# Optimization experiments

Hardware: AMD Instinct MI355X
Metric: run time of the kernel (lower is better)

Reference implementation:

```python
import jax, jax.numpy as jnp
import numpy as np

T, H = 1024, 2048          # tokens, hidden size
E, F = 32, 1408            # routed experts, expert intermediate
G, TOPK_G, TOPK = 8, 3, 6  # expert groups, top groups, top-k experts
FS = 2 * F                 # shared-expert intermediate (n_shared_experts=2)
SCALE = 16.0               # routed_scaling_factor


def setup_inputs() -> dict:
    key = jax.random.key(0)
    ks = jax.random.split(key, 6)
    s = 0.02
    return {
        "hidden_states": jax.random.normal(ks[0], (T, H), jnp.float32),
        "w_gate": jax.random.normal(ks[1], (E, H), jnp.float32) * s,
        "w1": jax.random.normal(ks[2], (E, H, 2 * F), jnp.float32) * s,   # gate_up per expert
        "w2": jax.random.normal(ks[3], (E, F, H), jnp.float32) * s,       # down per expert
        "ws1": jax.random.normal(ks[4], (H, 2 * FS), jnp.float32) * s,    # shared gate_up
        "ws2": jax.random.normal(ks[5], (FS, H), jnp.float32) * s,        # shared down
    }


def _grouped_topk(scores):
    # scores: [T, E] softmax probs. DeepSeek grouped top-k routing.
    g_scores = scores.reshape(T, G, E // G).max(axis=-1)          # [T, G]
    _, g_idx = jax.lax.top_k(g_scores, TOPK_G)                    # [T, TOPK_G]
    g_mask = jnp.zeros((T, G), scores.dtype).at[
        jnp.arange(T)[:, None], g_idx].set(1.0)                   # [T, G]
    score_mask = jnp.repeat(g_mask, E // G, axis=1)               # [T, E]
    masked = scores * score_mask                                  # masked_fill(0)
    topk_w, topk_ids = jax.lax.top_k(masked, TOPK)                # [T, TOPK]
    # norm_topk_prob=False -> no renormalization
    return topk_w, topk_ids


def reference(hidden_states, w_gate, w1, w2, ws1, ws2):
    x = hidden_states  # [T, H]

    # shared experts MLP (SiluAndMul)
    gu_s = x @ ws1                                   # [T, 2*FS]
    shared = (jax.nn.silu(gu_s[:, :FS]) * gu_s[:, FS:]) @ ws2  # [T, H]

    # router
    logits = x @ w_gate.T                            # [T, E]
    scores = jax.nn.softmax(logits, axis=-1)
    topk_w, topk_ids = _grouped_topk(scores)

    # combine weights as dense [T, E] (reference-dense expert execution)
    comb = jnp.zeros((T, E), x.dtype).at[
        jnp.arange(T)[:, None], topk_ids].add(topk_w)

    gu = jnp.einsum('th,ehf->tef', x, w1)            # [T, E, 2F]
    act = jax.nn.silu(gu[..., :F]) * gu[..., F:]     # [T, E, F]
    routed = jnp.einsum('tef,efh,te->th', act, w2, comb)  # weighted combine

    return routed * SCALE + shared
```

## Files before the change

### kernel.cpp

```cpp
#include <hip/hip_runtime.h>
#include <hip/hip_bf16.h>

#define T_TOK 1024
#define H_DIM 2048
#define E_NUM 32
#define F_DIM 1408
#define G_NUM 8
#define TOPKG 3
#define TOPK  6
#define FS_DIM 2816
#define SCALE_F 16.0f

#define BM 128
#define BK 32
#define LDP 40

typedef __attribute__((ext_vector_type(8))) __bf16 bf16x8;
typedef __attribute__((ext_vector_type(4))) float f32x4;

__device__ __forceinline__ unsigned short f2bf(float f) {
    union { float f; unsigned u; } v; v.f = f;
    unsigned r = v.u + 0x7fffu + ((v.u >> 16) & 1u);
    return (unsigned short)(r >> 16);
}

__device__ __forceinline__ bf16x8 ld_frag(const unsigned short* p) {
    union { uint4 u; bf16x8 v; } x;
    x.u = *(const uint4*)p;
    return x.v;
}

__device__ __forceinline__ f32x4 mfma16(bf16x8 a, bf16x8 b, f32x4 c) {
    return __builtin_amdgcn_mfma_f32_16x16x32_bf16(a, b, c, 0, 0, 0);
}

__global__ void prep_kernel(const float* __restrict__ x, unsigned short* __restrict__ xb,
                            int* __restrict__ cnt, int* __restrict__ cnt2) {
    if (blockIdx.x == 0) {
        if (threadIdx.x < E_NUM) cnt[threadIdx.x] = 0;
        else if (threadIdx.x < 2 * E_NUM) cnt2[threadIdx.x - E_NUM] = 0;
    }
    int i = blockIdx.x * blockDim.x + threadIdx.x;
    float4 v = ((const float4*)x)[i];
    uint2 o;
    o.x = (unsigned)f2bf(v.x) | ((unsigned)f2bf(v.y) << 16);
    o.y = (unsigned)f2bf(v.z) | ((unsigned)f2bf(v.w) << 16);
    ((uint2*)xb)[i] = o;
}

__global__ void router_kernel(const float* __restrict__ x, const float* __restrict__ wg,
                              float* __restrict__ topk_w, int* __restrict__ topk_ids,
                              int* __restrict__ cnt) {
    int t = blockIdx.x;
    __shared__ float xs[H_DIM];
    __shared__ float logits[E_NUM];
    const float* xr = x + (size_t)t * H_DIM;
    for (int i = threadIdx.x; i < H_DIM / 4; i += 256)
        ((float4*)xs)[i] = ((const float4*)xr)[i];
    __syncthreads();
    int wave = threadIdx.x >> 6, lane = threadIdx.x & 63;
    for (int eo = 0; eo < 8; ++eo) {
        int e = wave * 8 + eo;
        const float* w = wg + (size_t)e * H_DIM;
        float s = 0.f;
        for (int i = lane; i < H_DIM; i += 64) s += xs[i] * w[i];
        for (int d = 32; d; d >>= 1) s += __shfl_down(s, d);
        if (lane == 0) logits[e] = s;
    }
    __syncthreads();
    if (threadIdx.x == 0) {
        float sc[E_NUM];
        float mx = -1e30f;
        for (int e = 0; e < E_NUM; ++e) mx = fmaxf(mx, logits[e]);
        float sum = 0.f;
        for (int e = 0; e < E_NUM; ++e) { sc[e] = expf(logits[e] - mx); sum += sc[e]; }
        float inv = 1.0f / sum;
        for (int e = 0; e < E_NUM; ++e) sc[e] *= inv;
        float gs[G_NUM];
        for (int g = 0; g < G_NUM; ++g) {
            float m = sc[g * 4];
            for (int j = 1; j < 4; ++j) m = fmaxf(m, sc[g * 4 + j]);
            gs[g] = m;
        }
        unsigned gmask = 0;
        for (int r = 0; r < TOPKG; ++r) {
            int best = 0; float bv = -1e30f;
            for (int g = 0; g < G_NUM; ++g)
                if (!((gmask >> g) & 1) && gs[g] > bv) { bv = gs[g]; best = g; }
            gmask |= 1u << best;
        }
        for (int e = 0; e < E_NUM; ++e)
            if (!((gmask >> (e >> 2)) & 1)) sc[e] = -1.0f;
        for (int r = 0; r < TOPK; ++r) {
            int best = 0; float bv = -1e30f;
            for (int e = 0; e < E_NUM; ++e)
                if (sc[e] > bv) { bv = sc[e]; best = e; }
            topk_w[t * TOPK + r] = bv;
            topk_ids[t * TOPK + r] = best;
            sc[best] = -2.0f;
            atomicAdd(&cnt[best], 1);
        }
    }
}

__global__ void scan_kernel(const int* __restrict__ cnt, int* __restrict__ off) {
    if (threadIdx.x == 0) {
        int a = 0;
        for (int e = 0; e < E_NUM; ++e) { off[e] = a; a += cnt[e]; }
        off[E_NUM] = a;
    }
}

__global__ void scatter_kernel(const int* __restrict__ topk_ids, const float* __restrict__ topk_w,
                               const int* __restrict__ off, int* __restrict__ cnt2,
                               int* __restrict__ perm_token, float* __restrict__ perm_w,
                               int* __restrict__ dest) {
    int i = blockIdx.x * blockDim.x + threadIdx.x;
    if (i >= T_TOK * TOPK) return;
    int t = i / TOPK;
    int e = topk_ids[i];
    float w = topk_w[i];
    int pos = off[e] + atomicAdd(&cnt2[e], 1);
    perm_token[pos] = t;
    perm_w[pos] = w * SCALE_F;
    dest[pos] = i;
}

template<bool ROUTED>
__global__ __launch_bounds__(256, 2)
void gate_up_kernel(const unsigned short* __restrict__ xb, const float* __restrict__ Bw,
                    unsigned short* __restrict__ act, const int* __restrict__ perm_token,
                    const int* __restrict__ off, int N2, int Fdim) {
    int e = ROUTED ? blockIdx.z : 0;
    int s0 = 0, M = T_TOK;
    if (ROUTED) { s0 = off[e]; M = off[e + 1] - s0; }
    int mbase = blockIdx.y * BM;
    if (mbase >= M) return;
    int nb = blockIdx.x * 64;
    const float* Bp = Bw + (size_t)e * H_DIM * N2;

    __shared__ unsigned short As[BM * LDP];
    __shared__ unsigned short Bs[128 * LDP];

    int tid = threadIdx.x;
    int lane = tid & 63;
    int wv = tid >> 6;
    int wm = wv >> 1, wn = wv & 1;
    int quad = lane >> 4;
    int l16 = lane & 15;

    f32x4 acc[4][4];
#pragma unroll
    for (int i = 0; i < 4; ++i)
#pragma unroll
        for (int j = 0; j < 4; ++j) acc[i][j] = (f32x4){0.f, 0.f, 0.f, 0.f};

    int ar = tid >> 2;
    int aseg = tid & 3;
    int bn = tid & 127;
    int bk0 = (tid >> 7) * 16;
    int bcol = (bn < 64) ? (nb + bn) : (nb + Fdim + (bn - 64));

    int tokA[2];
#pragma unroll
    for (int i = 0; i < 2; ++i) {
        int g = mbase + i * 64 + ar;
        tokA[i] = (g < M) ? (ROUTED ? perm_token[s0 + g] : g) : -1;
    }

    for (int k0 = 0; k0 < H_DIM; k0 += BK) {
#pragma unroll
        for (int i = 0; i < 2; ++i) {
            int r = i * 64 + ar;
            uint4 v = {0u, 0u, 0u, 0u};
            if (tokA[i] >= 0)
                v = *(const uint4*)(xb + (size_t)tokA[i] * H_DIM + k0 + aseg * 8);
            *(uint4*)(&As[r * LDP + aseg * 8]) = v;
        }
        {
            const float* bp = Bp + (size_t)(k0 + bk0) * N2 + bcol;
            float f[16];
#pragma unroll
            for (int j = 0; j < 16; ++j) f[j] = bp[(size_t)j * N2];
            uint4 w0, w1v;
            w0.x = (unsigned)f2bf(f[0]) | ((unsigned)f2bf(f[1]) << 16);
            w0.y = (unsigned)f2bf(f[2]) | ((unsigned)f2bf(f[3]) << 16);
            w0.z = (unsigned)f2bf(f[4]) | ((unsigned)f2bf(f[5]) << 16);
            w0.w = (unsigned)f2bf(f[6]) | ((unsigned)f2bf(f[7]) << 16);
            w1v.x = (unsigned)f2bf(f[8]) | ((unsigned)f2bf(f[9]) << 16);
            w1v.y = (unsigned)f2bf(f[10]) | ((unsigned)f2bf(f[11]) << 16);
            w1v.z = (unsigned)f2bf(f[12]) | ((unsigned)f2bf(f[13]) << 16);
            w1v.w = (unsigned)f2bf(f[14]) | ((unsigned)f2bf(f[15]) << 16);
            *(uint4*)(&Bs[bn * LDP + bk0]) = w0;
            *(uint4*)(&Bs[bn * LDP + bk0 + 8]) = w1v;
        }
        __syncthreads();
        bf16x8 af[4], bfr[4];
#pragma unroll
        for (int i = 0; i < 4; ++i) {
            int m = wm * 64 + i * 16 + l16;
            af[i] = ld_frag(&As[m * LDP + quad * 8]);
        }
#pragma unroll
        for (int j = 0; j < 4; ++j) {
            int n = (j < 2) ? (wn * 32 + j * 16 + l16) : (64 + wn * 32 + (j - 2) * 16 + l16);
            bfr[j] = ld_frag(&Bs[n * LDP + quad * 8]);
        }
#pragma unroll
        for (int i = 0; i < 4; ++i)
#pragma unroll
            for (int j = 0; j < 4; ++j)
                acc[i][j] = mfma16(af[i], bfr[j], acc[i][j]);
        __syncthreads();
    }

#pragma unroll
    for (int i = 0; i < 4; ++i) {
#pragma unroll
        for (int j = 0; j < 2; ++j) {
            f32x4 aL = acc[i][j], aR = acc[i][j + 2];
            int col = nb + wn * 32 + j * 16 + l16;
#pragma unroll
            for (int r = 0; r < 4; ++r) {
                int row = wm * 64 + i * 16 + quad * 4 + r;
                int g = mbase + row;
                if (g < M) {
                    float L = aL[r];
                    float s = L / (1.0f + __expf(-L));
                    act[(size_t)(s0 + g) * Fdim + col] = f2bf(s * aR[r]);
                }
            }
        }
    }
}

template<bool ROUTED>
__global__ __launch_bounds__(256, 2)
void down_kernel(const unsigned short* __restrict__ act, const float* __restrict__ Bw,
                 float* __restrict__ outp, const float* __restrict__ perm_w,
                 const int* __restrict__ dest, const int* __restrict__ off, int K) {
    int e = ROUTED ? blockIdx.z : 0;
    int s0 = 0, M = T_TOK;
    if (ROUTED) { s0 = off[e]; M = off[e + 1] - s0; }
    int mbase = blockIdx.y * BM;
    if (mbase >= M) return;
    int nb = blockIdx.x * 128;
    const float* Bp = Bw + (size_t)e * K * H_DIM;

    __shared__ unsigned short As[BM * LDP];
    __shared__ unsigned short Bs[128 * LDP];

    int tid = threadIdx.x;
    int lane = tid & 63;
    int wv = tid >> 6;
    int wm = wv >> 1, wn = wv & 1;
    int quad = lane >> 4;
    int l16 = lane & 15;

    f32x4 acc[4][4];
#pragma unroll
    for (int i = 0; i < 4; ++i)
#pragma unroll
        for (int j = 0; j < 4; ++j) acc[i][j] = (f32x4){0.f, 0.f, 0.f, 0.f};

    int ar = tid >> 2;
    int aseg = tid & 3;
    int bn = tid & 127;
    int bk0 = (tid >> 7) * 16;
    int bcol = nb + bn;

    for (int k0 = 0; k0 < K; k0 += BK) {
#pragma unroll
        for (int i = 0; i < 2; ++i) {
            int r = i * 64 + ar;
            int g = mbase + r;
            uint4 v = {0u, 0u, 0u, 0u};
            if (g < M)
                v = *(const uint4*)(act + (size_t)(s0 + g) * K + k0 + aseg * 8);
            *(uint4*)(&As[r * LDP + aseg * 8]) = v;
        }
        {
            const float* bp = Bp + (size_t)(k0 + bk0) * H_DIM + bcol;
            float f[16];
#pragma unroll
            for (int j = 0; j < 16; ++j) f[j] = bp[(size_t)j * H_DIM];
            uint4 w0, w1v;
            w0.x = (unsigned)f2bf(f[0]) | ((unsigned)f2bf(f[1]) << 16);
            w0.y = (unsigned)f2bf(f[2]) | ((unsigned)f2bf(f[3]) << 16);
            w0.z = (unsigned)f2bf(f[4]) | ((unsigned)f2bf(f[5]) << 16);
            w0.w = (unsigned)f2bf(f[6]) | ((unsigned)f2bf(f[7]) << 16);
            w1v.x = (unsigned)f2bf(f[8]) | ((unsigned)f2bf(f[9]) << 16);
            w1v.y = (unsigned)f2bf(f[10]) | ((unsigned)f2bf(f[11]) << 16);
            w1v.z = (unsigned)f2bf(f[12]) | ((unsigned)f2bf(f[13]) << 16);
            w1v.w = (unsigned)f2bf(f[14]) | ((unsigned)f2bf(f[15]) << 16);
            *(uint4*)(&Bs[bn * LDP + bk0]) = w0;
            *(uint4*)(&Bs[bn * LDP + bk0 + 8]) = w1v;
        }
        __syncthreads();
        bf16x8 af[4], bfr[4];
#pragma unroll
        for (int i = 0; i < 4; ++i) {
            int m = wm * 64 + i * 16 + l16;
            af[i] = ld_frag(&As[m * LDP + quad * 8]);
        }
#pragma unroll
        for (int j = 0; j < 4; ++j) {
            int n = wn * 64 + j * 16 + l16;
            bfr[j] = ld_frag(&Bs[n * LDP + quad * 8]);
        }
#pragma unroll
        for (int i = 0; i < 4; ++i)
#pragma unroll
            for (int j = 0; j < 4; ++j)
                acc[i][j] = mfma16(af[i], bfr[j], acc[i][j]);
        __syncthreads();
    }

#pragma unroll
    for (int i = 0; i < 4; ++i) {
#pragma unroll
        for (int j = 0; j < 4; ++j) {
            int col = nb + wn * 64 + j * 16 + l16;
#pragma unroll
            for (int r = 0; r < 4; ++r) {
                int row = wm * 64 + i * 16 + quad * 4 + r;
                int g = mbase + row;
                if (g < M) {
                    float w = ROUTED ? perm_w[s0 + g] : 1.0f;
                    int drow = ROUTED ? dest[s0 + g] : g;
                    outp[(size_t)drow * H_DIM + col] = acc[i][j][r] * w;
                }
            }
        }
    }
}

__global__ void combine_kernel(float* __restrict__ outp, const float* __restrict__ partial) {
    int t = blockIdx.x;
    const float4* p0 = (const float4*)(partial + (size_t)t * TOPK * H_DIM);
    float4* o = (float4*)(outp + (size_t)t * H_DIM);
    for (int i = threadIdx.x; i < H_DIM / 4; i += 256) {
        float4 v = o[i];
#pragma unroll
        for (int k = 0; k < TOPK; ++k) {
            float4 p = p0[(size_t)k * (H_DIM / 4) + i];
            v.x += p.x; v.y += p.y; v.z += p.z; v.w += p.w;
        }
        o[i] = v;
    }
}

extern "C" void kernel_launch(void* const* d_in, const int* in_sizes, int n_in,
                              void* d_out, int out_size, void* d_ws, size_t ws_size,
                              hipStream_t stream) {
    const float* x   = (const float*)d_in[0];
    const float* wg  = (const float*)d_in[1];
    const float* w1  = (const float*)d_in[2];
    const float* w2  = (const float*)d_in[3];
    const float* ws1 = (const float*)d_in[4];
    const float* ws2 = (const float*)d_in[5];
    float* out = (float*)d_out;

    char* p = (char*)d_ws;
    auto alloc = [&](size_t bytes) {
        char* r = p;
        p += (bytes + 255) & ~(size_t)255;
        return r;
    };
    unsigned short* xb      = (unsigned short*)alloc((size_t)T_TOK * H_DIM * 2);
    float*          topk_w  = (float*)alloc((size_t)T_TOK * TOPK * 4);
    int*            topkid  = (int*)alloc((size_t)T_TOK * TOPK * 4);
    int*            cnt     = (int*)alloc(E_NUM * 4);
    int*            cnt2    = (int*)alloc(E_NUM * 4);
    int*            offs    = (int*)alloc((E_NUM + 1) * 4);
    int*            permtok = (int*)alloc((size_t)T_TOK * TOPK * 4);
    float*          permw   = (float*)alloc((size_t)T_TOK * TOPK * 4);
    int*            dest    = (int*)alloc((size_t)T_TOK * TOPK * 4);
    unsigned short* act_r   = (unsigned short*)alloc((size_t)T_TOK * TOPK * F_DIM * 2);
    unsigned short* act_s   = (unsigned short*)alloc((size_t)T_TOK * FS_DIM * 2);
    float*          partial = (float*)alloc((size_t)T_TOK * TOPK * H_DIM * 4);

    prep_kernel<<<(T_TOK * H_DIM / 4) / 256, 256, 0, stream>>>(x, xb, cnt, cnt2);
    router_kernel<<<T_TOK, 256, 0, stream>>>(x, wg, topk_w, topkid, cnt);
    scan_kernel<<<1, 64, 0, stream>>>(cnt, offs);
    scatter_kernel<<<(T_TOK * TOPK + 255) / 256, 256, 0, stream>>>(topkid, topk_w, offs, cnt2,
                                                                   permtok, permw, dest);
    gate_up_kernel<true><<<dim3(F_DIM / 64, T_TOK / BM, E_NUM), 256, 0, stream>>>(
        xb, w1, act_r, permtok, offs, 2 * F_DIM, F_DIM);
    gate_up_kernel<false><<<dim3(FS_DIM / 64, T_TOK / BM, 1), 256, 0, stream>>>(
        xb, ws1, act_s, nullptr, nullptr, 2 * FS_DIM, FS_DIM);
    down_kernel<false><<<dim3(H_DIM / 128, T_TOK / BM, 1), 256, 0, stream>>>(
        act_s, ws2, out, nullptr, nullptr, nullptr, FS_DIM);
    down_kernel<true><<<dim3(H_DIM / 128, T_TOK / BM, E_NUM), 256, 0, stream>>>(
        act_r, w2, partial, permw, dest, offs, F_DIM);
    combine_kernel<<<T_TOK, 256, 0, stream>>>(out, partial);
}
```

Baseline: 1.677 ms.

## Use 512-thread 256-row GEMM tiles with direct global-to-LDS A-tile loads

The gate_up and down GEMM kernels move to 512 threads with 256-row M tiles, which halves how often each weight tile is reloaded and converted across M blocks. The activation (A) tile is loaded straight into LDS with global_load_lds, bypassing registers, and the LDS padding is dropped. Weight conversion now uses a byte-perm pack, and dimensions become template parameters. Removing the padding may bring LDS bank conflicts, and the larger tiles leave fewer blocks for small experts.

```diff
diff --git a/kernel.cpp b/kernel.cpp
--- a/kernel.cpp
+++ b/kernel.cpp
@@ -11,9 +11,8 @@
 #define FS_DIM 2816
 #define SCALE_F 16.0f
 
-#define BM 128
+#define BM 256
 #define BK 32
-#define LDP 40
 
 typedef __attribute__((ext_vector_type(8))) __bf16 bf16x8;
 typedef __attribute__((ext_vector_type(4))) float f32x4;
@@ -24,6 +23,13 @@
     return (unsigned short)(r >> 16);
 }
 
+__device__ __forceinline__ unsigned pk2(float a, float b) {
+    union { float f; unsigned u; } x, y; x.f = a; y.f = b;
+    unsigned ra = x.u + 0x7fffu + ((x.u >> 16) & 1u);
+    unsigned rb = y.u + 0x7fffu + ((y.u >> 16) & 1u);
+    return __builtin_amdgcn_perm(rb, ra, 0x07060302);
+}
+
 __device__ __forceinline__ bf16x8 ld_frag(const unsigned short* p) {
     union { uint4 u; bf16x8 v; } x;
     x.u = *(const uint4*)p;
@@ -32,6 +38,12 @@
 
 __device__ __forceinline__ f32x4 mfma16(bf16x8 a, bf16x8 b, f32x4 c) {
     return __builtin_amdgcn_mfma_f32_16x16x32_bf16(a, b, c, 0, 0, 0);
+}
+
+__device__ __forceinline__ void gload_lds16(const void* g, void* l) {
+    __builtin_amdgcn_global_load_lds(
+        (const __attribute__((address_space(1))) unsigned int*)g,
+        (__attribute__((address_space(3))) unsigned int*)l, 16, 0, 0);
 }
 
 __global__ void prep_kernel(const float* __restrict__ x, unsigned short* __restrict__ xb,
@@ -126,21 +138,22 @@
     dest[pos] = i;
 }
 
-template<bool ROUTED>
-__global__ __launch_bounds__(256, 2)
+template<bool ROUTED, int N2, int FD>
+__global__ __launch_bounds__(512, 4)
 void gate_up_kernel(const unsigned short* __restrict__ xb, const float* __restrict__ Bw,
                     unsigned short* __restrict__ act, const int* __restrict__ perm_token,
-                    const int* __restrict__ off, int N2, int Fdim) {
+                    const int* __restrict__ off) {
     int e = ROUTED ? blockIdx.z : 0;
+    int nb = blockIdx.x * 64;
+    if (nb >= FD) return;
     int s0 = 0, M = T_TOK;
     if (ROUTED) { s0 = off[e]; M = off[e + 1] - s0; }
     int mbase = blockIdx.y * BM;
     if (mbase >= M) return;
-    int nb = blockIdx.x * 64;
     const float* Bp = Bw + (size_t)e * H_DIM * N2;
 
-    __shared__ unsigned short As[BM * LDP];
-    __shared__ unsigned short Bs[128 * LDP];
+    __shared__ unsigned short As[256 * 32];
+    __shared__ unsigned short Bs[128 * 32];
 
     int tid = threadIdx.x;
     int lane = tid & 63;
@@ -155,90 +168,86 @@
 #pragma unroll
         for (int j = 0; j < 4; ++j) acc[i][j] = (f32x4){0.f, 0.f, 0.f, 0.f};
 
-    int ar = tid >> 2;
-    int aseg = tid & 3;
+    const unsigned short* aSrc0;
+    const unsigned short* aSrc1;
+    {
+        int g0 = mbase + (tid >> 2);
+        int g1 = g0 + 128;
+        int t0, t1;
+        if (ROUTED) {
+            t0 = perm_token[s0 + ((g0 < M) ? g0 : 0)];
+            t1 = perm_token[s0 + ((g1 < M) ? g1 : 0)];
+        } else {
+            t0 = (g0 < M) ? g0 : 0;
+            t1 = (g1 < M) ? g1 : 0;
+        }
+        aSrc0 = xb + (size_t)t0 * H_DIM + (tid & 3) * 8;
+        aSrc1 = xb + (size_t)t1 * H_DIM + (tid & 3) * 8;
+    }
+    char* aDst0 = (char*)As + tid * 16;
+    char* aDst1 = (char*)As + 8192 + tid * 16;
+
     int bn = tid & 127;
-    int bk0 = (tid >> 7) * 16;
-    int bcol = (bn < 64) ? (nb + bn) : (nb + Fdim + (bn - 64));
-
-    int tokA[2];
-#pragma unroll
-    for (int i = 0; i < 2; ++i) {
-        int g = mbase + i * 64 + ar;
-        tokA[i] = (g < M) ? (ROUTED ? perm_token[s0 + g] : g) : -1;
-    }
+    int bk0 = (tid >> 7) * 8;
+    int bcol = (bn < 64) ? (nb + bn) : (FD + nb + (bn - 64));
+    const float* bSrc = Bp + (size_t)bk0 * N2 + bcol;
+    uint4* bDst = (uint4*)(&Bs[bn * 32 + bk0]);
 
     for (int k0 = 0; k0 < H_DIM; k0 += BK) {
-#pragma unroll
-        for (int i = 0; i < 2; ++i) {
-            int r = i * 64 + ar;
-            uint4 v = {0u, 0u, 0u, 0u};
-            if (tokA[i] >= 0)
-                v = *(const uint4*)(xb + (size_t)tokA[i] * H_DIM + k0 + aseg * 8);
-            *(uint4*)(&As[r * LDP + aseg * 8]) = v;
-        }
+        gload_lds16(aSrc0 + k0, aDst0);
+        gload_lds16(aSrc1 + k0, aDst1);
         {
-            const float* bp = Bp + (size_t)(k0 + bk0) * N2 + bcol;
-            float f[16];
-#pragma unroll
-            for (int j = 0; j < 16; ++j) f[j] = bp[(size_t)j * N2];
-            uint4 w0, w1v;
-            w0.x = (unsigned)f2bf(f[0]) | ((unsigned)f2bf(f[1]) << 16);
-            w0.y = (unsigned)f2bf(f[2]) | ((unsigned)f2bf(f[3]) << 16);
-            w0.z = (unsigned)f2bf(f[4]) | ((unsigned)f2bf(f[5]) << 16);
-            w0.w = (unsigned)f2bf(f[6]) | ((unsigned)f2bf(f[7]) << 16);
-            w1v.x = (unsigned)f2bf(f[8]) | ((unsigned)f2bf(f[9]) << 16);
-            w1v.y = (unsigned)f2bf(f[10]) | ((unsigned)f2bf(f[11]) << 16);
-            w1v.z = (unsigned)f2bf(f[12]) | ((unsigned)f2bf(f[13]) << 16);
-            w1v.w = (unsigned)f2bf(f[14]) | ((unsigned)f2bf(f[15]) << 16);
-            *(uint4*)(&Bs[bn * LDP + bk0]) = w0;
-            *(uint4*)(&Bs[bn * LDP + bk0 + 8]) = w1v;
-        }
+            float f0 = bSrc[0 * (size_t)N2], f1 = bSrc[1 * (size_t)N2];
+            float f2 = bSrc[2 * (size_t)N2], f3 = bSrc[3 * (size_t)N2];
+            float f4 = bSrc[4 * (size_t)N2], f5 = bSrc[5 * (size_t)N2];
+            float f6 = bSrc[6 * (size_t)N2], f7 = bSrc[7 * (size_t)N2];
+            uint4 w;
+            w.x = pk2(f0, f1); w.y = pk2(f2, f3);
+            w.z = pk2(f4, f5); w.w = pk2(f6, f7);
+            *bDst = w;
+        }
+        bSrc += (size_t)BK * N2;
         __syncthreads();
-        bf16x8 af[4], bfr[4];
-#pragma unroll
-        for (int i = 0; i < 4; ++i) {
-            int m = wm * 64 + i * 16 + l16;
-            af[i] = ld_frag(&As[m * LDP + quad * 8]);
-        }
+        bf16x8 af[4];
+#pragma unroll
+        for (int i = 0; i < 4; ++i)
+            af[i] = ld_frag(&As[(wm * 64 + i * 16 + l16) * 32 + quad * 8]);
 #pragma unroll
         for (int j = 0; j < 4; ++j) {
             int n = (j < 2) ? (wn * 32 + j * 16 + l16) : (64 + wn * 32 + (j - 2) * 16 + l16);
-            bfr[j] = ld_frag(&Bs[n * LDP + quad * 8]);
-        }
-#pragma unroll
-        for (int i = 0; i < 4; ++i)
-#pragma unroll
-            for (int j = 0; j < 4; ++j)
-                acc[i][j] = mfma16(af[i], bfr[j], acc[i][j]);
+            bf16x8 bfr = ld_frag(&Bs[n * 32 + quad * 8]);
+#pragma unroll
+            for (int i = 0; i < 4; ++i)
+                acc[i][j] = mfma16(af[i], bfr, acc[i][j]);
+        }
         __syncthreads();
     }
 
 #pragma unroll
     for (int i = 0; i < 4; ++i) {
 #pragma unroll
-        for (int j = 0; j < 2; ++j) {
-            f32x4 aL = acc[i][j], aR = acc[i][j + 2];
-            int col = nb + wn * 32 + j * 16 + l16;
-#pragma unroll
-            for (int r = 0; r < 4; ++r) {
-                int row = wm * 64 + i * 16 + quad * 4 + r;
-                int g = mbase + row;
-                if (g < M) {
-                    float L = aL[r];
+        for (int r = 0; r < 4; ++r) {
+            int row = wm * 64 + i * 16 + quad * 4 + r;
+            int g = mbase + row;
+            if (g < M) {
+                unsigned short* ap = act + (size_t)(s0 + g) * FD + nb + wn * 32 + l16;
+#pragma unroll
+                for (int j = 0; j < 2; ++j) {
+                    float L = acc[i][j][r];
+                    float R = acc[i][j + 2][r];
                     float s = L / (1.0f + __expf(-L));
-                    act[(size_t)(s0 + g) * Fdim + col] = f2bf(s * aR[r]);
+                    ap[j * 16] = f2bf(s * R);
                 }
             }
         }
     }
 }
 
-template<bool ROUTED>
-__global__ __launch_bounds__(256, 2)
+template<bool ROUTED, int K>
+__global__ __launch_bounds__(512, 4)
 void down_kernel(const unsigned short* __restrict__ act, const float* __restrict__ Bw,
                  float* __restrict__ outp, const float* __restrict__ perm_w,
-                 const int* __restrict__ dest, const int* __restrict__ off, int K) {
+                 const int* __restrict__ dest, const int* __restrict__ off) {
     int e = ROUTED ? blockIdx.z : 0;
     int s0 = 0, M = T_TOK;
     if (ROUTED) { s0 = off[e]; M = off[e + 1] - s0; }
@@ -247,8 +256,8 @@
     int nb = blockIdx.x * 128;
     const float* Bp = Bw + (size_t)e * K * H_DIM;
 
-    __shared__ unsigned short As[BM * LDP];
-    __shared__ unsigned short Bs[128 * LDP];
+    __shared__ unsigned short As[256 * 32];
+    __shared__ unsigned short Bs[128 * 32];
 
     int tid = threadIdx.x;
     int lane = tid & 63;
@@ -263,73 +272,67 @@
 #pragma unroll
         for (int j = 0; j < 4; ++j) acc[i][j] = (f32x4){0.f, 0.f, 0.f, 0.f};
 
-    int ar = tid >> 2;
-    int aseg = tid & 3;
+    const unsigned short* aSrc0;
+    const unsigned short* aSrc1;
+    {
+        int g0 = mbase + (tid >> 2);
+        int g1 = g0 + 128;
+        int r0 = s0 + ((g0 < M) ? g0 : 0);
+        int r1 = s0 + ((g1 < M) ? g1 : 0);
+        aSrc0 = act + (size_t)r0 * K + (tid & 3) * 8;
+        aSrc1 = act + (size_t)r1 * K + (tid & 3) * 8;
+    }
+    char* aDst0 = (char*)As + tid * 16;
+    char* aDst1 = (char*)As + 8192 + tid * 16;
+
     int bn = tid & 127;
-    int bk0 = (tid >> 7) * 16;
-    int bcol = nb + bn;
+    int bk0 = (tid >> 7) * 8;
+    const float* bSrc = Bp + (size_t)bk0 * H_DIM + nb + bn;
+    uint4* bDst = (uint4*)(&Bs[bn * 32 + bk0]);
 
     for (int k0 = 0; k0 < K; k0 += BK) {
-#pragma unroll
-        for (int i = 0; i < 2; ++i) {
-            int r = i * 64 + ar;
-            int g = mbase + r;
-            uint4 v = {0u, 0u, 0u, 0u};
-            if (g < M)
-                v = *(const uint4*)(act + (size_t)(s0 + g) * K + k0 + aseg * 8);
-            *(uint4*)(&As[r * LDP + aseg * 8]) = v;
-        }
+        gload_lds16(aSrc0 + k0, aDst0);
+        gload_lds16(aSrc1 + k0, aDst1);
         {
-            const float* bp = Bp + (size_t)(k0 + bk0) * H_DIM + bcol;
-            float f[16];
-#pragma unroll
-            for (int j = 0; j < 16; ++j) f[j] = bp[(size_t)j * H_DIM];
-            uint4 w0, w1v;
-            w0.x = (unsigned)f2bf(f[0]) | ((unsigned)f2bf(f[1]) << 16);
-            w0.y = (unsigned)f2bf(f[2]) | ((unsigned)f2bf(f[3]) << 16);
-            w0.z = (unsigned)f2bf(f[4]) | ((unsigned)f2bf(f[5]) << 16);
-            w0.w = (unsigned)f2bf(f[6]) | ((unsigned)f2bf(f[7]) << 16);
-            w1v.x = (unsigned)f2bf(f[8]) | ((unsigned)f2bf(f[9]) << 16);
-            w1v.y = (unsigned)f2bf(f[10]) | ((unsigned)f2bf(f[11]) << 16);
-            w1v.z = (unsigned)f2bf(f[12]) | ((unsigned)f2bf(f[13]) << 16);
-            w1v.w = (unsigned)f2bf(f[14]) | ((unsigned)f2bf(f[15]) << 16);
-            *(uint4*)(&Bs[bn * LDP + bk0]) = w0;
-            *(uint4*)(&Bs[bn * LDP + bk0 + 8]) = w1v;
-        }
+            float f0 = bSrc[0 * (size_t)H_DIM], f1 = bSrc[1 * (size_t)H_DIM];
+            float f2 = bSrc[2 * (size_t)H_DIM], f3 = bSrc[3 * (size_t)H_DIM];
+            float f4 = bSrc[4 * (size_t)H_DIM], f5 = bSrc[5 * (size_t)H_DIM];
+            float f6 = bSrc[6 * (size_t)H_DIM], f7 = bSrc[7 * (size_t)H_DIM];
+            uint4 w;
+            w.x = pk2(f0, f1); w.y = pk2(f2, f3);
+            w.z = pk2(f4, f5); w.w = pk2(f6, f7);
+            *bDst = w;
+        }
+        bSrc += (size_t)BK * H_DIM;
         __syncthreads();
-        bf16x8 af[4], bfr[4];
-#pragma unroll
-        for (int i = 0; i < 4; ++i) {
-            int m = wm * 64 + i * 16 + l16;
-            af[i] = ld_frag(&As[m * LDP + quad * 8]);
-        }
+        bf16x8 af[4];
+#pragma unroll
+        for (int i = 0; i < 4; ++i)
+            af[i] = ld_frag(&As[(wm * 64 + i * 16 + l16) * 32 + quad * 8]);
 #pragma unroll
         for (int j = 0; j < 4; ++j) {
             int n = wn * 64 + j * 16 + l16;
-            bfr[j] = ld_frag(&Bs[n * LDP + quad * 8]);
-        }
-#pragma unroll
-        for (int i = 0; i < 4; ++i)
-#pragma unroll
-            for (int j = 0; j < 4; ++j)
-                acc[i][j] = mfma16(af[i], bfr[j], acc[i][j]);
+            bf16x8 bfr = ld_frag(&Bs[n * 32 + quad * 8]);
+#pragma unroll
+            for (int i = 0; i < 4; ++i)
+                acc[i][j] = mfma16(af[i], bfr, acc[i][j]);
+        }
         __syncthreads();
     }
 
 #pragma unroll
     for (int i = 0; i < 4; ++i) {
 #pragma unroll
-        for (int j = 0; j < 4; ++j) {
-            int col = nb + wn * 64 + j * 16 + l16;
-#pragma unroll
-            for (int r = 0; r < 4; ++r) {
-                int row = wm * 64 + i * 16 + quad * 4 + r;
-                int g = mbase + row;
-                if (g < M) {
-                    float w = ROUTED ? perm_w[s0 + g] : 1.0f;
-                    int drow = ROUTED ? dest[s0 + g] : g;
-                    outp[(size_t)drow * H_DIM + col] = acc[i][j][r] * w;
-                }
+        for (int r = 0; r < 4; ++r) {
+            int row = wm * 64 + i * 16 + quad * 4 + r;
+            int g = mbase + row;
+            if (g < M) {
+                float w = ROUTED ? perm_w[s0 + g] : 1.0f;
+                int drow = ROUTED ? dest[s0 + g] : g;
+                float* op = outp + (size_t)drow * H_DIM + nb + wn * 64 + l16;
+#pragma unroll
+                for (int j = 0; j < 4; ++j)
+                    op[j * 16] = acc[i][j][r] * w;
             }
         }
     }
@@ -385,13 +388,13 @@
     scan_kernel<<<1, 64, 0, stream>>>(cnt, offs);
     scatter_kernel<<<(T_TOK * TOPK + 255) / 256, 256, 0, stream>>>(topkid, topk_w, offs, cnt2,
                                                                    permtok, permw, dest);
-    gate_up_kernel<true><<<dim3(F_DIM / 64, T_TOK / BM, E_NUM), 256, 0, stream>>>(
-        xb, w1, act_r, permtok, offs, 2 * F_DIM, F_DIM);
-    gate_up_kernel<false><<<dim3(FS_DIM / 64, T_TOK / BM, 1), 256, 0, stream>>>(
-        xb, ws1, act_s, nullptr, nullptr, 2 * FS_DIM, FS_DIM);
-    down_kernel<false><<<dim3(H_DIM / 128, T_TOK / BM, 1), 256, 0, stream>>>(
-        act_s, ws2, out, nullptr, nullptr, nullptr, FS_DIM);
-    down_kernel<true><<<dim3(H_DIM / 128, T_TOK / BM, E_NUM), 256, 0, stream>>>(
-        act_r, w2, partial, permw, dest, offs, F_DIM);
+    gate_up_kernel<true, 2 * F_DIM, F_DIM><<<dim3(24, 4, E_NUM), 512, 0, stream>>>(
+        xb, w1, act_r, permtok, offs);
+    gate_up_kernel<false, 2 * FS_DIM, FS_DIM><<<dim3(48, 4, 1), 512, 0, stream>>>(
+        xb, ws1, act_s, nullptr, nullptr);
+    down_kernel<false, FS_DIM><<<dim3(16, 4, 1), 512, 0, stream>>>(
+        act_s, ws2, out, nullptr, nullptr, nullptr);
+    down_kernel<true, F_DIM><<<dim3(16, 4, E_NUM), 512, 0, stream>>>(
+        act_r, w2, partial, permw, dest, offs);
     combine_kernel<<<T_TOK, 256, 0, stream>>>(out, partial);
 }
```

Result: slower. 1.867 ms (+11.3%).
